# Performance work log

Hardware: AMD Instinct MI355X
Metric: run time of the kernel (lower is better)

The kernel has to match this reference:

```python
import jax, jax.numpy as jnp
import numpy as np

N = 100000   # nodes
E = 1600000  # edges
IN = 32
HID = 64
OUT = 1

def setup_inputs() -> dict:
    key = jax.random.key(0)
    ks = jax.random.split(key, 16)
    x = jax.random.normal(ks[0], (N, IN), jnp.float32)
    edge_index = jax.random.randint(ks[1], (2, E), 0, N, dtype=jnp.int32)
    def lin(k, fi, fo):
        return jax.random.normal(k, (fi, fo), jnp.float32) / np.sqrt(fi)
    # SAGEConv params per layer: Wn/bn for aggregated neighbors (lin_l), Wr for root (lin_r, no bias)
    Wn0 = lin(ks[2], IN, HID);  bn0 = jnp.zeros((HID,), jnp.float32); Wr0 = lin(ks[3], IN, HID)
    Wn1 = lin(ks[4], HID, HID); bn1 = jnp.zeros((HID,), jnp.float32); Wr1 = lin(ks[5], HID, HID)
    Wn2 = lin(ks[6], HID, HID); bn2 = jnp.zeros((HID,), jnp.float32); Wr2 = lin(ks[7], HID, HID)
    # predictor MLP
    Wp1 = lin(ks[8], HID, HID); bp1 = jnp.zeros((HID,), jnp.float32)
    Wp2 = lin(ks[9], HID, OUT); bp2 = jnp.zeros((OUT,), jnp.float32)
    return dict(x=x, edge_index=edge_index,
                Wn0=Wn0, bn0=bn0, Wr0=Wr0,
                Wn1=Wn1, bn1=bn1, Wr1=Wr1,
                Wn2=Wn2, bn2=bn2, Wr2=Wr2,
                Wp1=Wp1, bp1=bp1, Wp2=Wp2, bp2=bp2)

def reference(x, edge_index, Wn0, bn0, Wr0, Wn1, bn1, Wr1, Wn2, bn2, Wr2, Wp1, bp1, Wp2, bp2):
    src, dst = edge_index[0], edge_index[1]
    n = x.shape[0]
    # mean-aggregation normalization (nodes with no in-edges get 0, as in PyG)
    cnt = jax.ops.segment_sum(jnp.ones(src.shape, x.dtype), dst, num_segments=n)
    inv = jnp.where(cnt > 0, 1.0 / jnp.maximum(cnt, 1.0), 0.0)[:, None]

    def sage(h, Wn, bn, Wr):
        agg = jax.ops.segment_sum(h[src], dst, num_segments=n) * inv  # [N, d]
        return agg @ Wn + bn + h @ Wr

    h = jax.nn.relu(sage(x, Wn0, bn0, Wr0))
    h = jax.nn.relu(sage(h, Wn1, bn1, Wr1))
    h = sage(h, Wn2, bn2, Wr2)  # no activation after last GNN layer
    h = jax.nn.relu(h @ Wp1 + bp1)
    return jax.nn.sigmoid(h @ Wp2 + bp2)
```

## Files before the change

kernel.cpp:

```cpp
#include <hip/hip_runtime.h>
#include <math.h>

#define NN 100000
#define EE 1600000
#define HID 64
#define BKT 391
#define SLAB 5504
#define CHUNK 4096
#define NWG ((EE + CHUNK - 1) / CHUNK)

typedef _Float16 f16;
typedef _Float16 f16x2 __attribute__((ext_vector_type(2)));

__device__ __forceinline__ f16x2 u2h(unsigned u) { return __builtin_bit_cast(f16x2, u); }
__device__ __forceinline__ unsigned h2u(f16x2 h) { return __builtin_bit_cast(unsigned, h); }

#if defined(__has_builtin) && __has_builtin(__builtin_amdgcn_fdot2)
__device__ __forceinline__ float dot2(f16x2 a, f16x2 b, float c) {
    return __builtin_amdgcn_fdot2(a, b, c, false);
}
#else
__device__ __forceinline__ float dot2(f16x2 a, f16x2 b, float c) {
    c = fmaf((float)a.x, (float)b.x, c);
    return fmaf((float)a.y, (float)b.y, c);
}
#endif


__global__ void place_kernel(const int* __restrict__ src, const int* __restrict__ dst,
                             int* __restrict__ bfill, unsigned* __restrict__ pairs) {
    __shared__ int lc[BKT];
    __shared__ int lbase[BKT];
    int t = threadIdx.x;
    for (int b = t; b < BKT; b += 256) lc[b] = 0;
    __syncthreads();
    int base = blockIdx.x * CHUNK;
    int myd[CHUNK / 256];
#pragma unroll
    for (int j = 0; j < CHUNK / 256; ++j) {
        int i = base + j * 256 + t;
        myd[j] = (i < EE) ? dst[i] : -1;
        if (myd[j] >= 0) atomicAdd(&lc[myd[j] >> 8], 1);
    }
    __syncthreads();
    for (int b = t; b < BKT; b += 256) {
        int c = lc[b];
        if (c) {
            int ofs = atomicAdd(&bfill[b], c);
            if (ofs + c > SLAB) ofs = SLAB - c;
            lbase[b] = b * SLAB + ofs;
        }
    }
    __syncthreads();
    for (int b = t; b < BKT; b += 256) lc[b] = 0;
    __syncthreads();
#pragma unroll
    for (int j = 0; j < CHUNK / 256; ++j) {
        int i = base + j * 256 + t;
        if (myd[j] >= 0) {
            int b = myd[j] >> 8;
            int r = atomicAdd(&lc[b], 1);
            pairs[lbase[b] + r] = (unsigned)src[i] | ((unsigned)(myd[j] & 255) << 24);
        }
    }
}

__global__ void build_kernel(const unsigned* __restrict__ pairs,
                             const int* __restrict__ bfill,
                             int* __restrict__ rs, int* __restrict__ re,
                             float* __restrict__ inv, int* __restrict__ col) {
    __shared__ unsigned s_pk[SLAB];
    __shared__ int ncnt[256];
    __shared__ int nexcl[256];
    int b = blockIdx.x;
    int t = threadIdx.x;
    int s0 = b * SLAB;
    int ce = bfill[b]; if (ce > SLAB) ce = SLAB;
    ncnt[t] = 0;
    for (int e = t; e < ce; e += 256) s_pk[e] = pairs[s0 + e];
    __syncthreads();
    for (int e = t; e < ce; e += 256) atomicAdd(&ncnt[s_pk[e] >> 24], 1);
    __syncthreads();
    int c = ncnt[t];
    nexcl[t] = c;
    __syncthreads();
    for (int off = 1; off < 256; off <<= 1) {
        int u = (t >= off) ? nexcl[t - off] : 0;
        __syncthreads();
        nexcl[t] += u;
        __syncthreads();
    }
    int excl = nexcl[t] - c;
    int node = (b << 8) + t;
    if (node < NN) {
        rs[node] = s0 + excl;
        re[node] = s0 + excl + c;
        inv[node] = (c > 0) ? (1.0f / (float)c) : 0.0f;
    }
    __syncthreads();
    nexcl[t] = excl;
    ncnt[t] = 0;
    __syncthreads();
    for (int e = t; e < ce; e += 256) {
        unsigned pk = s_pk[e];
        int d = pk >> 24;
        int r = atomicAdd(&ncnt[d], 1);
        col[s0 + nexcl[d] + r] = (int)(pk & 0xFFFFFFu);
    }
}


__global__ void transform32_kernel(const float* __restrict__ h,
                                   const float* __restrict__ Wn,
                                   const float* __restrict__ bn,
                                   const float* __restrict__ Wr,
                                   f16* __restrict__ hn,
                                   f16* __restrict__ hrb,
                                   const float* __restrict__ Wn1,
                                   const float* __restrict__ Wr1,
                                   const float* __restrict__ Wn2,
                                   const float* __restrict__ Wr2,
                                   const float* __restrict__ Wp1,
                                   unsigned* __restrict__ w16) {
    if (blockIdx.x < 40) {
        int id = blockIdx.x * 256 + threadIdx.x;
        int mat = id >> 11;
        int p = (id >> 6) & 31;
        int j = id & 63;
        const float* W = (mat == 0) ? Wn1 : (mat == 1) ? Wr1 :
                         (mat == 2) ? Wn2 : (mat == 3) ? Wr2 : Wp1;
        f16x2 v;
        v.x = (f16)W[(2 * p) * HID + j];
        v.y = (f16)W[(2 * p + 1) * HID + j];
        w16[id] = h2u(v);
    }

    int lane = threadIdx.x & 63;
    int wid = (blockIdx.x * blockDim.x + threadIdx.x) >> 6;
    int m0 = __builtin_amdgcn_readfirstlane(wid << 2);
    const float* h0 = h + (size_t)m0 * 32;

    float an0 = 0.f, an1 = 0.f, an2 = 0.f, an3 = 0.f;
    float ar0 = 0.f, ar1 = 0.f, ar2 = 0.f, ar3 = 0.f;
#pragma unroll
    for (int k = 0; k < 32; ++k) {
        float wn = Wn[k * HID + lane];
        float wr = Wr[k * HID + lane];
        float hk0 = h0[k], hk1 = h0[32 + k], hk2 = h0[64 + k], hk3 = h0[96 + k];
        an0 = fmaf(hk0, wn, an0); ar0 = fmaf(hk0, wr, ar0);
        an1 = fmaf(hk1, wn, an1); ar1 = fmaf(hk1, wr, ar1);
        an2 = fmaf(hk2, wn, an2); ar2 = fmaf(hk2, wr, ar2);
        an3 = fmaf(hk3, wn, an3); ar3 = fmaf(hk3, wr, ar3);
    }
    float b = bn[lane];
    size_t o = (size_t)m0 * HID + lane;
    hn[o] = (f16)an0; hn[o + HID] = (f16)an1;
    hn[o + 2 * HID] = (f16)an2; hn[o + 3 * HID] = (f16)an3;
    hrb[o] = (f16)(ar0 + b); hrb[o + HID] = (f16)(ar1 + b);
    hrb[o + 2 * HID] = (f16)(ar2 + b); hrb[o + 3 * HID] = (f16)(ar3 + b);
}


__device__ __forceinline__ void qgather(const uint2* __restrict__ rp,
                                        const int* __restrict__ col,
                                        int e, int en, int fl,
                                        float& a0, float& a1, float& a2, float& a3) {
    while (e + 8 <= en) {
        int c0 = col[e],     c1 = col[e + 1], c2 = col[e + 2], c3 = col[e + 3];
        int c4 = col[e + 4], c5 = col[e + 5], c6 = col[e + 6], c7 = col[e + 7];
        uint2 v0 = rp[(size_t)c0 * 16 + fl];
        uint2 v1 = rp[(size_t)c1 * 16 + fl];
        uint2 v2 = rp[(size_t)c2 * 16 + fl];
        uint2 v3 = rp[(size_t)c3 * 16 + fl];
        uint2 v4 = rp[(size_t)c4 * 16 + fl];
        uint2 v5 = rp[(size_t)c5 * 16 + fl];
        uint2 v6 = rp[(size_t)c6 * 16 + fl];
        uint2 v7 = rp[(size_t)c7 * 16 + fl];
        f16x2 pa, pb;
        pa = u2h(v0.x); pb = u2h(v0.y); a0 += (float)pa.x; a1 += (float)pa.y; a2 += (float)pb.x; a3 += (float)pb.y;
        pa = u2h(v1.x); pb = u2h(v1.y); a0 += (float)pa.x; a1 += (float)pa.y; a2 += (float)pb.x; a3 += (float)pb.y;
        pa = u2h(v2.x); pb = u2h(v2.y); a0 += (float)pa.x; a1 += (float)pa.y; a2 += (float)pb.x; a3 += (float)pb.y;
        pa = u2h(v3.x); pb = u2h(v3.y); a0 += (float)pa.x; a1 += (float)pa.y; a2 += (float)pb.x; a3 += (float)pb.y;
        pa = u2h(v4.x); pb = u2h(v4.y); a0 += (float)pa.x; a1 += (float)pa.y; a2 += (float)pb.x; a3 += (float)pb.y;
        pa = u2h(v5.x); pb = u2h(v5.y); a0 += (float)pa.x; a1 += (float)pa.y; a2 += (float)pb.x; a3 += (float)pb.y;
        pa = u2h(v6.x); pb = u2h(v6.y); a0 += (float)pa.x; a1 += (float)pa.y; a2 += (float)pb.x; a3 += (float)pb.y;
        pa = u2h(v7.x); pb = u2h(v7.y); a0 += (float)pa.x; a1 += (float)pa.y; a2 += (float)pb.x; a3 += (float)pb.y;
        e += 8;
    }
    if (e + 4 <= en) {
        int c0 = col[e], c1 = col[e + 1], c2 = col[e + 2], c3 = col[e + 3];
        uint2 v0 = rp[(size_t)c0 * 16 + fl];
        uint2 v1 = rp[(size_t)c1 * 16 + fl];
        uint2 v2 = rp[(size_t)c2 * 16 + fl];
        uint2 v3 = rp[(size_t)c3 * 16 + fl];
        f16x2 pa, pb;
        pa = u2h(v0.x); pb = u2h(v0.y); a0 += (float)pa.x; a1 += (float)pa.y; a2 += (float)pb.x; a3 += (float)pb.y;
        pa = u2h(v1.x); pb = u2h(v1.y); a0 += (float)pa.x; a1 += (float)pa.y; a2 += (float)pb.x; a3 += (float)pb.y;
        pa = u2h(v2.x); pb = u2h(v2.y); a0 += (float)pa.x; a1 += (float)pa.y; a2 += (float)pb.x; a3 += (float)pb.y;
        pa = u2h(v3.x); pb = u2h(v3.y); a0 += (float)pa.x; a1 += (float)pa.y; a2 += (float)pb.x; a3 += (float)pb.y;
        e += 4;
    }
    while (e < en) {
        uint2 v = rp[(size_t)col[e] * 16 + fl];
        f16x2 pa = u2h(v.x), pb = u2h(v.y);
        a0 += (float)pa.x; a1 += (float)pa.y; a2 += (float)pb.x; a3 += (float)pb.y;
        ++e;
    }
}


__global__ void gt_kernel(const f16* __restrict__ An,
                          const int* __restrict__ rs, const int* __restrict__ re,
                          const int* __restrict__ col, const float* __restrict__ inv,
                          f16* C,
                          const unsigned* __restrict__ Wn16, const float* __restrict__ bn,
                          const unsigned* __restrict__ Wr16,
                          f16* __restrict__ Aout) {
    int lane = threadIdx.x & 63;
    int wid = (blockIdx.x * blockDim.x + threadIdx.x) >> 6;
    int m0 = wid << 2;
    int m = m0 + (lane >> 4);
    int fl = lane & 15;

    float a0 = 0.f, a1 = 0.f, a2 = 0.f, a3 = 0.f;
    qgather((const uint2*)An, col, rs[m], re[m], fl, a0, a1, a2, a3);

    float iv = inv[m];
    uint2 cur = ((const uint2*)C)[(size_t)m * 16 + fl];
    f16x2 q0 = u2h(cur.x), q1 = u2h(cur.y);
    f16x2 hA, hB;
    hA.x = (f16)fmaxf(fmaf(a0, iv, (float)q0.x), 0.f);
    hA.y = (f16)fmaxf(fmaf(a1, iv, (float)q0.y), 0.f);
    hB.x = (f16)fmaxf(fmaf(a2, iv, (float)q1.x), 0.f);
    hB.y = (f16)fmaxf(fmaf(a3, iv, (float)q1.y), 0.f);
    unsigned hx = h2u(hA), hy = h2u(hB);

    float an[4] = {0.f, 0.f, 0.f, 0.f};
    float ar[4] = {0.f, 0.f, 0.f, 0.f};
#pragma unroll
    for (int kk = 0; kk < 16; ++kk) {
        f16x2 wnA = u2h(Wn16[(2 * kk) * HID + lane]);
        f16x2 wnB = u2h(Wn16[(2 * kk + 1) * HID + lane]);
        f16x2 wrA = u2h(Wr16[(2 * kk) * HID + lane]);
        f16x2 wrB = u2h(Wr16[(2 * kk + 1) * HID + lane]);
#pragma unroll
        for (int n = 0; n < 4; ++n) {
            f16x2 px = u2h(__shfl(hx, (n << 4) + kk));
            f16x2 py = u2h(__shfl(hy, (n << 4) + kk));
            an[n] = dot2(px, wnA, an[n]);
            an[n] = dot2(py, wnB, an[n]);
            ar[n] = dot2(px, wrA, ar[n]);
            ar[n] = dot2(py, wrB, ar[n]);
        }
    }
    float b = bn[lane];
    size_t o = (size_t)m0 * HID + lane;
#pragma unroll
    for (int n = 0; n < 4; ++n) {
        Aout[o + n * HID] = (f16)an[n];
        C[o + n * HID] = (f16)(ar[n] + b);
    }
}


__global__ void gh_kernel(const f16* __restrict__ An,
                          const int* __restrict__ rs, const int* __restrict__ re,
                          const int* __restrict__ col, const float* __restrict__ inv,
                          const f16* __restrict__ C,
                          const unsigned* __restrict__ Wp116, const float* __restrict__ bp1,
                          const float* __restrict__ Wp2, const float* __restrict__ bp2,
                          float* __restrict__ out) {
    int lane = threadIdx.x & 63;
    int wid = (blockIdx.x * blockDim.x + threadIdx.x) >> 6;
    int m0 = wid << 2;
    int m = m0 + (lane >> 4);
    int fl = lane & 15;

    float a0 = 0.f, a1 = 0.f, a2 = 0.f, a3 = 0.f;
    qgather((const uint2*)An, col, rs[m], re[m], fl, a0, a1, a2, a3);

    float iv = inv[m];
    uint2 cur = ((const uint2*)C)[(size_t)m * 16 + fl];
    f16x2 q0 = u2h(cur.x), q1 = u2h(cur.y);
    f16x2 hA, hB;
    hA.x = (f16)fmaf(a0, iv, (float)q0.x);
    hA.y = (f16)fmaf(a1, iv, (float)q0.y);
    hB.x = (f16)fmaf(a2, iv, (float)q1.x);
    hB.y = (f16)fmaf(a3, iv, (float)q1.y);
    unsigned hx = h2u(hA), hy = h2u(hB);

    float tn[4] = {0.f, 0.f, 0.f, 0.f};
#pragma unroll
    for (int kk = 0; kk < 16; ++kk) {
        f16x2 wA = u2h(Wp116[(2 * kk) * HID + lane]);
        f16x2 wB = u2h(Wp116[(2 * kk + 1) * HID + lane]);
#pragma unroll
        for (int n = 0; n < 4; ++n) {
            f16x2 px = u2h(__shfl(hx, (n << 4) + kk));
            f16x2 py = u2h(__shfl(hy, (n << 4) + kk));
            tn[n] = dot2(px, wA, tn[n]);
            tn[n] = dot2(py, wB, tn[n]);
        }
    }
    float b = bp1[lane], w2v = Wp2[lane];
    float r0 = fmaxf(tn[0] + b, 0.f) * w2v;
    float r1 = fmaxf(tn[1] + b, 0.f) * w2v;
    float r2 = fmaxf(tn[2] + b, 0.f) * w2v;
    float r3 = fmaxf(tn[3] + b, 0.f) * w2v;
#pragma unroll
    for (int off = 32; off > 0; off >>= 1) {
        r0 += __shfl_xor(r0, off);
        r1 += __shfl_xor(r1, off);
        r2 += __shfl_xor(r2, off);
        r3 += __shfl_xor(r3, off);
    }
    if (lane == 0) {
        float bb = bp2[0];
        out[m0]     = 1.f / (1.f + expf(-(r0 + bb)));
        out[m0 + 1] = 1.f / (1.f + expf(-(r1 + bb)));
        out[m0 + 2] = 1.f / (1.f + expf(-(r2 + bb)));
        out[m0 + 3] = 1.f / (1.f + expf(-(r3 + bb)));
    }
}

extern "C" void kernel_launch(void* const* d_in, const int* in_sizes, int n_in,
                              void* d_out, int out_size, void* d_ws, size_t ws_size,
                              hipStream_t stream) {
    const float* x   = (const float*)d_in[0];
    const int* eidx  = (const int*)d_in[1];
    const float* Wn0 = (const float*)d_in[2];
    const float* bn0 = (const float*)d_in[3];
    const float* Wr0 = (const float*)d_in[4];
    const float* Wn1 = (const float*)d_in[5];
    const float* bn1 = (const float*)d_in[6];
    const float* Wr1 = (const float*)d_in[7];
    const float* Wn2 = (const float*)d_in[8];
    const float* bn2 = (const float*)d_in[9];
    const float* Wr2 = (const float*)d_in[10];
    const float* Wp1 = (const float*)d_in[11];
    const float* bp1 = (const float*)d_in[12];
    const float* Wp2 = (const float*)d_in[13];
    const float* bp2 = (const float*)d_in[14];
    float* out = (float*)d_out;

    const int* src = eidx;
    const int* dst = eidx + EE;

    char* w = (char*)d_ws;
    size_t off = 0;
    auto carve = [&](size_t bytes) -> void* {
        void* p = w + off;
        off = (off + bytes + 255) & ~(size_t)255;
        return p;
    };
    int*   rsA    = (int*)carve((size_t)NN * 4);
    int*   reA    = (int*)carve((size_t)NN * 4);
    float* inv    = (float*)carve((size_t)NN * 4);
    int*   col    = (int*)carve((size_t)BKT * SLAB * 4);
    int*   bfill  = (int*)carve((size_t)BKT * 4);
    unsigned* w16 = (unsigned*)carve((size_t)5 * 2048 * 4);
    f16*   A0     = (f16*)carve((size_t)NN * HID * 2);
    f16*   A1     = (f16*)carve((size_t)NN * HID * 2);
    f16*   C      = (f16*)carve((size_t)NN * HID * 2);
    unsigned* pairs = (unsigned*)carve((size_t)BKT * SLAB * 4);
    (void)ws_size;

    unsigned* Wn1_16 = w16;
    unsigned* Wr1_16 = w16 + 2048;
    unsigned* Wn2_16 = w16 + 4096;
    unsigned* Wr2_16 = w16 + 6144;
    unsigned* Wp1_16 = w16 + 8192;

    hipMemsetAsync(bfill, 0, (size_t)BKT * 4, stream);

    place_kernel<<<NWG, 256, 0, stream>>>(src, dst, bfill, pairs);
    build_kernel<<<BKT, 256, 0, stream>>>(pairs, bfill, rsA, reA, inv, col);

    const int tb = NN / 16;

    transform32_kernel<<<tb, 256, 0, stream>>>(x, Wn0, bn0, Wr0, A0, C,
                                               Wn1, Wr1, Wn2, Wr2, Wp1, w16);
    gt_kernel<<<tb, 256, 0, stream>>>(A0, rsA, reA, col, inv, C, Wn1_16, bn1, Wr1_16, A1);
    gt_kernel<<<tb, 256, 0, stream>>>(A1, rsA, reA, col, inv, C, Wn2_16, bn2, Wr2_16, A0);
    gh_kernel<<<tb, 256, 0, stream>>>(A0, rsA, reA, col, inv, C, Wp1_16, bp1, Wp2, bp2, out);
}
```

Measured before the change: 289.3 us.

## Gather 16-byte rows with 8 lanes per node and accumulate in packed fp16

The neighbor gather now uses uint4 (16-byte) loads with 8 lanes per node, so each wave handles 8 nodes instead of 4. The per-node transform loops are restructured to match. Neighbor sums are accumulated in packed f16x2 instead of fp32, which removes the per-element conversions and halves the accumulate instructions. The intent is fewer, wider memory requests and more rows in flight per wave; in exchange, fp16 accumulation over many neighbors loses precision and risks overflow, and the grid has half as many blocks.

```diff
diff --git a/kernel.cpp b/kernel.cpp
--- a/kernel.cpp
+++ b/kernel.cpp
@@ -161,49 +161,46 @@
 }
 
 
-__device__ __forceinline__ void qgather(const uint2* __restrict__ rp,
+__device__ __forceinline__ void ogather(const uint4* __restrict__ rp,
                                         const int* __restrict__ col,
                                         int e, int en, int fl,
-                                        float& a0, float& a1, float& a2, float& a3) {
+                                        f16x2& s0, f16x2& s1, f16x2& s2, f16x2& s3) {
     while (e + 8 <= en) {
         int c0 = col[e],     c1 = col[e + 1], c2 = col[e + 2], c3 = col[e + 3];
         int c4 = col[e + 4], c5 = col[e + 5], c6 = col[e + 6], c7 = col[e + 7];
-        uint2 v0 = rp[(size_t)c0 * 16 + fl];
-        uint2 v1 = rp[(size_t)c1 * 16 + fl];
-        uint2 v2 = rp[(size_t)c2 * 16 + fl];
-        uint2 v3 = rp[(size_t)c3 * 16 + fl];
-        uint2 v4 = rp[(size_t)c4 * 16 + fl];
-        uint2 v5 = rp[(size_t)c5 * 16 + fl];
-        uint2 v6 = rp[(size_t)c6 * 16 + fl];
-        uint2 v7 = rp[(size_t)c7 * 16 + fl];
-        f16x2 pa, pb;
-        pa = u2h(v0.x); pb = u2h(v0.y); a0 += (float)pa.x; a1 += (float)pa.y; a2 += (float)pb.x; a3 += (float)pb.y;
-        pa = u2h(v1.x); pb = u2h(v1.y); a0 += (float)pa.x; a1 += (float)pa.y; a2 += (float)pb.x; a3 += (float)pb.y;
-        pa = u2h(v2.x); pb = u2h(v2.y); a0 += (float)pa.x; a1 += (float)pa.y; a2 += (float)pb.x; a3 += (float)pb.y;
-        pa = u2h(v3.x); pb = u2h(v3.y); a0 += (float)pa.x; a1 += (float)pa.y; a2 += (float)pb.x; a3 += (float)pb.y;
-        pa = u2h(v4.x); pb = u2h(v4.y); a0 += (float)pa.x; a1 += (float)pa.y; a2 += (float)pb.x; a3 += (float)pb.y;
-        pa = u2h(v5.x); pb = u2h(v5.y); a0 += (float)pa.x; a1 += (float)pa.y; a2 += (float)pb.x; a3 += (float)pb.y;
-        pa = u2h(v6.x); pb = u2h(v6.y); a0 += (float)pa.x; a1 += (float)pa.y; a2 += (float)pb.x; a3 += (float)pb.y;
-        pa = u2h(v7.x); pb = u2h(v7.y); a0 += (float)pa.x; a1 += (float)pa.y; a2 += (float)pb.x; a3 += (float)pb.y;
+        uint4 v0 = rp[(size_t)c0 * 8 + fl];
+        uint4 v1 = rp[(size_t)c1 * 8 + fl];
+        uint4 v2 = rp[(size_t)c2 * 8 + fl];
+        uint4 v3 = rp[(size_t)c3 * 8 + fl];
+        uint4 v4 = rp[(size_t)c4 * 8 + fl];
+        uint4 v5 = rp[(size_t)c5 * 8 + fl];
+        uint4 v6 = rp[(size_t)c6 * 8 + fl];
+        uint4 v7 = rp[(size_t)c7 * 8 + fl];
+        s0 += u2h(v0.x); s1 += u2h(v0.y); s2 += u2h(v0.z); s3 += u2h(v0.w);
+        s0 += u2h(v1.x); s1 += u2h(v1.y); s2 += u2h(v1.z); s3 += u2h(v1.w);
+        s0 += u2h(v2.x); s1 += u2h(v2.y); s2 += u2h(v2.z); s3 += u2h(v2.w);
+        s0 += u2h(v3.x); s1 += u2h(v3.y); s2 += u2h(v3.z); s3 += u2h(v3.w);
+        s0 += u2h(v4.x); s1 += u2h(v4.y); s2 += u2h(v4.z); s3 += u2h(v4.w);
+        s0 += u2h(v5.x); s1 += u2h(v5.y); s2 += u2h(v5.z); s3 += u2h(v5.w);
+        s0 += u2h(v6.x); s1 += u2h(v6.y); s2 += u2h(v6.z); s3 += u2h(v6.w);
+        s0 += u2h(v7.x); s1 += u2h(v7.y); s2 += u2h(v7.z); s3 += u2h(v7.w);
         e += 8;
     }
     if (e + 4 <= en) {
         int c0 = col[e], c1 = col[e + 1], c2 = col[e + 2], c3 = col[e + 3];
-        uint2 v0 = rp[(size_t)c0 * 16 + fl];
-        uint2 v1 = rp[(size_t)c1 * 16 + fl];
-        uint2 v2 = rp[(size_t)c2 * 16 + fl];
-        uint2 v3 = rp[(size_t)c3 * 16 + fl];
-        f16x2 pa, pb;
-        pa = u2h(v0.x); pb = u2h(v0.y); a0 += (float)pa.x; a1 += (float)pa.y; a2 += (float)pb.x; a3 += (float)pb.y;
-        pa = u2h(v1.x); pb = u2h(v1.y); a0 += (float)pa.x; a1 += (float)pa.y; a2 += (float)pb.x; a3 += (float)pb.y;
-        pa = u2h(v2.x); pb = u2h(v2.y); a0 += (float)pa.x; a1 += (float)pa.y; a2 += (float)pb.x; a3 += (float)pb.y;
-        pa = u2h(v3.x); pb = u2h(v3.y); a0 += (float)pa.x; a1 += (float)pa.y; a2 += (float)pb.x; a3 += (float)pb.y;
+        uint4 v0 = rp[(size_t)c0 * 8 + fl];
+        uint4 v1 = rp[(size_t)c1 * 8 + fl];
+        uint4 v2 = rp[(size_t)c2 * 8 + fl];
+        uint4 v3 = rp[(size_t)c3 * 8 + fl];
+        s0 += u2h(v0.x); s1 += u2h(v0.y); s2 += u2h(v0.z); s3 += u2h(v0.w);
+        s0 += u2h(v1.x); s1 += u2h(v1.y); s2 += u2h(v1.z); s3 += u2h(v1.w);
+        s0 += u2h(v2.x); s1 += u2h(v2.y); s2 += u2h(v2.z); s3 += u2h(v2.w);
+        s0 += u2h(v3.x); s1 += u2h(v3.y); s2 += u2h(v3.z); s3 += u2h(v3.w);
         e += 4;
     }
     while (e < en) {
-        uint2 v = rp[(size_t)col[e] * 16 + fl];
-        f16x2 pa = u2h(v.x), pb = u2h(v.y);
-        a0 += (float)pa.x; a1 += (float)pa.y; a2 += (float)pb.x; a3 += (float)pb.y;
+        uint4 v = rp[(size_t)col[e] * 8 + fl];
+        s0 += u2h(v.x); s1 += u2h(v.y); s2 += u2h(v.z); s3 += u2h(v.w);
         ++e;
     }
 }
@@ -218,45 +215,56 @@
                           f16* __restrict__ Aout) {
     int lane = threadIdx.x & 63;
     int wid = (blockIdx.x * blockDim.x + threadIdx.x) >> 6;
-    int m0 = wid << 2;
-    int m = m0 + (lane >> 4);
-    int fl = lane & 15;
-
-    float a0 = 0.f, a1 = 0.f, a2 = 0.f, a3 = 0.f;
-    qgather((const uint2*)An, col, rs[m], re[m], fl, a0, a1, a2, a3);
+    int m0 = wid << 3;
+    int m = m0 + (lane >> 3);
+    int fl = lane & 7;
+
+    f16x2 s0 = (f16x2)0, s1 = (f16x2)0, s2 = (f16x2)0, s3 = (f16x2)0;
+    ogather((const uint4*)An, col, rs[m], re[m], fl, s0, s1, s2, s3);
 
     float iv = inv[m];
-    uint2 cur = ((const uint2*)C)[(size_t)m * 16 + fl];
-    f16x2 q0 = u2h(cur.x), q1 = u2h(cur.y);
-    f16x2 hA, hB;
-    hA.x = (f16)fmaxf(fmaf(a0, iv, (float)q0.x), 0.f);
-    hA.y = (f16)fmaxf(fmaf(a1, iv, (float)q0.y), 0.f);
-    hB.x = (f16)fmaxf(fmaf(a2, iv, (float)q1.x), 0.f);
-    hB.y = (f16)fmaxf(fmaf(a3, iv, (float)q1.y), 0.f);
-    unsigned hx = h2u(hA), hy = h2u(hB);
-
-    float an[4] = {0.f, 0.f, 0.f, 0.f};
-    float ar[4] = {0.f, 0.f, 0.f, 0.f};
-#pragma unroll
-    for (int kk = 0; kk < 16; ++kk) {
-        f16x2 wnA = u2h(Wn16[(2 * kk) * HID + lane]);
-        f16x2 wnB = u2h(Wn16[(2 * kk + 1) * HID + lane]);
-        f16x2 wrA = u2h(Wr16[(2 * kk) * HID + lane]);
-        f16x2 wrB = u2h(Wr16[(2 * kk + 1) * HID + lane]);
-#pragma unroll
-        for (int n = 0; n < 4; ++n) {
-            f16x2 px = u2h(__shfl(hx, (n << 4) + kk));
-            f16x2 py = u2h(__shfl(hy, (n << 4) + kk));
-            an[n] = dot2(px, wnA, an[n]);
-            an[n] = dot2(py, wnB, an[n]);
-            ar[n] = dot2(px, wrA, ar[n]);
-            ar[n] = dot2(py, wrB, ar[n]);
+    uint4 cur = ((const uint4*)C)[(size_t)m * 8 + fl];
+    f16x2 q0 = u2h(cur.x), q1 = u2h(cur.y), q2 = u2h(cur.z), q3 = u2h(cur.w);
+    f16x2 hA, hB, hC, hD;
+    hA.x = (f16)fmaxf(fmaf((float)s0.x, iv, (float)q0.x), 0.f);
+    hA.y = (f16)fmaxf(fmaf((float)s0.y, iv, (float)q0.y), 0.f);
+    hB.x = (f16)fmaxf(fmaf((float)s1.x, iv, (float)q1.x), 0.f);
+    hB.y = (f16)fmaxf(fmaf((float)s1.y, iv, (float)q1.y), 0.f);
+    hC.x = (f16)fmaxf(fmaf((float)s2.x, iv, (float)q2.x), 0.f);
+    hC.y = (f16)fmaxf(fmaf((float)s2.y, iv, (float)q2.y), 0.f);
+    hD.x = (f16)fmaxf(fmaf((float)s3.x, iv, (float)q3.x), 0.f);
+    hD.y = (f16)fmaxf(fmaf((float)s3.y, iv, (float)q3.y), 0.f);
+    unsigned h0 = h2u(hA), h1 = h2u(hB), h2 = h2u(hC), h3 = h2u(hD);
+
+    float an[8] = {0.f, 0.f, 0.f, 0.f, 0.f, 0.f, 0.f, 0.f};
+    float ar[8] = {0.f, 0.f, 0.f, 0.f, 0.f, 0.f, 0.f, 0.f};
+#pragma unroll
+    for (int kk = 0; kk < 8; ++kk) {
+        f16x2 wn0 = u2h(Wn16[(4 * kk) * HID + lane]);
+        f16x2 wn1 = u2h(Wn16[(4 * kk + 1) * HID + lane]);
+        f16x2 wn2 = u2h(Wn16[(4 * kk + 2) * HID + lane]);
+        f16x2 wn3 = u2h(Wn16[(4 * kk + 3) * HID + lane]);
+        f16x2 wr0 = u2h(Wr16[(4 * kk) * HID + lane]);
+        f16x2 wr1 = u2h(Wr16[(4 * kk + 1) * HID + lane]);
+        f16x2 wr2 = u2h(Wr16[(4 * kk + 2) * HID + lane]);
+        f16x2 wr3 = u2h(Wr16[(4 * kk + 3) * HID + lane]);
+#pragma unroll
+        for (int n = 0; n < 8; ++n) {
+            int sl = (n << 3) + kk;
+            f16x2 p0 = u2h(__shfl(h0, sl));
+            f16x2 p1 = u2h(__shfl(h1, sl));
+            f16x2 p2 = u2h(__shfl(h2, sl));
+            f16x2 p3 = u2h(__shfl(h3, sl));
+            an[n] = dot2(p0, wn0, an[n]); an[n] = dot2(p1, wn1, an[n]);
+            an[n] = dot2(p2, wn2, an[n]); an[n] = dot2(p3, wn3, an[n]);
+            ar[n] = dot2(p0, wr0, ar[n]); ar[n] = dot2(p1, wr1, ar[n]);
+            ar[n] = dot2(p2, wr2, ar[n]); ar[n] = dot2(p3, wr3, ar[n]);
         }
     }
     float b = bn[lane];
     size_t o = (size_t)m0 * HID + lane;
 #pragma unroll
-    for (int n = 0; n < 4; ++n) {
+    for (int n = 0; n < 8; ++n) {
         Aout[o + n * HID] = (f16)an[n];
         C[o + n * HID] = (f16)(ar[n] + b);
     }
@@ -272,54 +280,59 @@
                           float* __restrict__ out) {
     int lane = threadIdx.x & 63;
     int wid = (blockIdx.x * blockDim.x + threadIdx.x) >> 6;
-    int m0 = wid << 2;
-    int m = m0 + (lane >> 4);
-    int fl = lane & 15;
-
-    float a0 = 0.f, a1 = 0.f, a2 = 0.f, a3 = 0.f;
-    qgather((const uint2*)An, col, rs[m], re[m], fl, a0, a1, a2, a3);
+    int m0 = wid << 3;
+    int m = m0 + (lane >> 3);
+    int fl = lane & 7;
+
+    f16x2 s0 = (f16x2)0, s1 = (f16x2)0, s2 = (f16x2)0, s3 = (f16x2)0;
+    ogather((const uint4*)An, col, rs[m], re[m], fl, s0, s1, s2, s3);
 
     float iv = inv[m];
-    uint2 cur = ((const uint2*)C)[(size_t)m * 16 + fl];
-    f16x2 q0 = u2h(cur.x), q1 = u2h(cur.y);
-    f16x2 hA, hB;
-    hA.x = (f16)fmaf(a0, iv, (float)q0.x);
-    hA.y = (f16)fmaf(a1, iv, (float)q0.y);
-    hB.x = (f16)fmaf(a2, iv, (float)q1.x);
-    hB.y = (f16)fmaf(a3, iv, (float)q1.y);
-    unsigned hx = h2u(hA), hy = h2u(hB);
-
-    float tn[4] = {0.f, 0.f, 0.f, 0.f};
-#pragma unroll
-    for (int kk = 0; kk < 16; ++kk) {
-        f16x2 wA = u2h(Wp116[(2 * kk) * HID + lane]);
-        f16x2 wB = u2h(Wp116[(2 * kk + 1) * HID + lane]);
-#pragma unroll
-        for (int n = 0; n < 4; ++n) {
-            f16x2 px = u2h(__shfl(hx, (n << 4) + kk));
-            f16x2 py = u2h(__shfl(hy, (n << 4) + kk));
-            tn[n] = dot2(px, wA, tn[n]);
-            tn[n] = dot2(py, wB, tn[n]);
+    uint4 cur = ((const uint4*)C)[(size_t)m * 8 + fl];
+    f16x2 q0 = u2h(cur.x), q1 = u2h(cur.y), q2 = u2h(cur.z), q3 = u2h(cur.w);
+    f16x2 hA, hB, hC, hD;
+    hA.x = (f16)fmaf((float)s0.x, iv, (float)q0.x);
+    hA.y = (f16)fmaf((float)s0.y, iv, (float)q0.y);
+    hB.x = (f16)fmaf((float)s1.x, iv, (float)q1.x);
+    hB.y = (f16)fmaf((float)s1.y, iv, (float)q1.y);
+    hC.x = (f16)fmaf((float)s2.x, iv, (float)q2.x);
+    hC.y = (f16)fmaf((float)s2.y, iv, (float)q2.y);
+    hD.x = (f16)fmaf((float)s3.x, iv, (float)q3.x);
+    hD.y = (f16)fmaf((float)s3.y, iv, (float)q3.y);
+    unsigned h0 = h2u(hA), h1 = h2u(hB), h2 = h2u(hC), h3 = h2u(hD);
+
+    float tn[8] = {0.f, 0.f, 0.f, 0.f, 0.f, 0.f, 0.f, 0.f};
+#pragma unroll
+    for (int kk = 0; kk < 8; ++kk) {
+        f16x2 w0 = u2h(Wp116[(4 * kk) * HID + lane]);
+        f16x2 w1 = u2h(Wp116[(4 * kk + 1) * HID + lane]);
+        f16x2 w2 = u2h(Wp116[(4 * kk + 2) * HID + lane]);
+        f16x2 w3 = u2h(Wp116[(4 * kk + 3) * HID + lane]);
+#pragma unroll
+        for (int n = 0; n < 8; ++n) {
+            int sl = (n << 3) + kk;
+            f16x2 p0 = u2h(__shfl(h0, sl));
+            f16x2 p1 = u2h(__shfl(h1, sl));
+            f16x2 p2 = u2h(__shfl(h2, sl));
+            f16x2 p3 = u2h(__shfl(h3, sl));
+            tn[n] = dot2(p0, w0, tn[n]); tn[n] = dot2(p1, w1, tn[n]);
+            tn[n] = dot2(p2, w2, tn[n]); tn[n] = dot2(p3, w3, tn[n]);
         }
     }
     float b = bp1[lane], w2v = Wp2[lane];
-    float r0 = fmaxf(tn[0] + b, 0.f) * w2v;
-    float r1 = fmaxf(tn[1] + b, 0.f) * w2v;
-    float r2 = fmaxf(tn[2] + b, 0.f) * w2v;
-    float r3 = fmaxf(tn[3] + b, 0.f) * w2v;
+    float r[8];
+#pragma unroll
+    for (int n = 0; n < 8; ++n) r[n] = fmaxf(tn[n] + b, 0.f) * w2v;
 #pragma unroll
     for (int off = 32; off > 0; off >>= 1) {
-        r0 += __shfl_xor(r0, off);
-        r1 += __shfl_xor(r1, off);
-        r2 += __shfl_xor(r2, off);
-        r3 += __shfl_xor(r3, off);
+#pragma unroll
+        for (int n = 0; n < 8; ++n) r[n] += __shfl_xor(r[n], off);
     }
     if (lane == 0) {
         float bb = bp2[0];
-        out[m0]     = 1.f / (1.f + expf(-(r0 + bb)));
-        out[m0 + 1] = 1.f / (1.f + expf(-(r1 + bb)));
-        out[m0 + 2] = 1.f / (1.f + expf(-(r2 + bb)));
-        out[m0 + 3] = 1.f / (1.f + expf(-(r3 + bb)));
+#pragma unroll
+        for (int n = 0; n < 8; ++n)
+            out[m0 + n] = 1.f / (1.f + expf(-(r[n] + bb)));
     }
 }
 
@@ -377,10 +390,11 @@
     build_kernel<<<BKT, 256, 0, stream>>>(pairs, bfill, rsA, reA, inv, col);
 
     const int tb = NN / 16;
+    const int ob = NN / 32;
 
     transform32_kernel<<<tb, 256, 0, stream>>>(x, Wn0, bn0, Wr0, A0, C,
                                                Wn1, Wr1, Wn2, Wr2, Wp1, w16);
-    gt_kernel<<<tb, 256, 0, stream>>>(A0, rsA, reA, col, inv, C, Wn1_16, bn1, Wr1_16, A1);
-    gt_kernel<<<tb, 256, 0, stream>>>(A1, rsA, reA, col, inv, C, Wn2_16, bn2, Wr2_16, A0);
-    gh_kernel<<<tb, 256, 0, stream>>>(A0, rsA, reA, col, inv, C, Wp1_16, bp1, Wp2, bp2, out);
-}
+    gt_kernel<<<ob, 256, 0, stream>>>(A0, rsA, reA, col, inv, C, Wn1_16, bn1, Wr1_16, A1);
+    gt_kernel<<<ob, 256, 0, stream>>>(A1, rsA, reA, col, inv, C, Wn2_16, bn2, Wr2_16, A0);
+    gh_kernel<<<ob, 256, 0, stream>>>(A0, rsA, reA, col, inv, C, Wp1_16, bp1, Wp2, bp2, out);
+}
```

Result: slower. 305.3 us (+5.5%).
